# Optimization experiments

Hardware: AMD Instinct MI355X
Metric: run time of the kernel (lower is better)

Reference implementation:

```python
import jax, jax.numpy as jnp
import numpy as np

PATCH_NUM = 10  # self.patch_num divisor
TOP_N = 5


def _extract_patches(feat, ps):
    """feat: [1,C,H,W] -> [P, C*ps*ps] with P = (H-ps)*(W-ps), matching the
    original loop over h in range(H-ps), w in range(W-ps)."""
    C, H, W = feat.shape[1:]
    Hm, Wm = H - ps, W - ps
    shifts = [feat[0, :, i:i + Hm, j:j + Wm] for i in range(ps) for j in range(ps)]
    patches = jnp.stack(shifts, axis=1)          # [C, ps*ps, Hm, Wm]
    return patches.reshape(C * ps * ps, Hm * Wm).T  # [P, K], P index = h*Wm + w


def _scale_loss(src_f, tgt_f, pos, ps):
    C = src_f.shape[1]
    K = C * ps * ps
    patches = _extract_patches(src_f, ps)  # [P, K]

    def per_target(p):
        th, tw = p[0], p[1]
        tpatch = jax.lax.dynamic_slice(tgt_f, (0, 0, th, tw), (1, C, ps, ps)).reshape(K)
        dist = jnp.sum(jnp.abs(patches - tpatch), axis=1)  # [P] summed L1 per patch
        _, ids = jax.lax.top_k(-dist, TOP_N)                # 5 nearest patches
        sel = patches[ids]                                   # [TOP_N, K]
        # sum over top-n of mean-L1, each divided by top_n (as in original)
        return jnp.sum(jnp.mean(jnp.abs(sel - tpatch), axis=1)) / TOP_N

    # sequential map over the small number of target patches keeps peak memory
    # at one [P,K] abs-diff buffer per step
    return jnp.sum(jax.lax.map(per_target, pos))


def setup_inputs() -> dict:
    key = jax.random.key(0)
    k0, k1, k2, k3, k4, k5 = jax.random.split(key, 6)
    return {
        "src_f0": jax.random.normal(k0, (1, 64, 256, 256), dtype=jnp.float32),
        "tgt_f0": jax.random.normal(k1, (1, 64, 256, 256), dtype=jnp.float32),
        "src_f1": jax.random.normal(k2, (1, 128, 128, 128), dtype=jnp.float32),
        "tgt_f1": jax.random.normal(k3, (1, 128, 128, 128), dtype=jnp.float32),
        "pos0": jax.random.randint(k4, (10, 2), 0, 253, dtype=jnp.int32),
        "pos1": jax.random.randint(k5, (5, 2), 0, 127, dtype=jnp.int32),
    }


def reference(src_f0, tgt_f0, src_f1, tgt_f1, pos0, pos1):
    loss = _scale_loss(src_f0, tgt_f0, pos0, 3) + _scale_loss(src_f1, tgt_f1, pos1, 1)
    return loss / PATCH_NUM
```

## Files before the change

### kernel.cpp

```cpp
#include <hip/hip_runtime.h>
#include <hip/hip_bf16.h>

#define BIG 3.4e38f


__device__ __forceinline__ void merge5(float a[5], const float* b) {
    float r[5];
#pragma unroll
    for (int k = 0; k < 5; ++k) {
        float best = BIG;
#pragma unroll
        for (int i = 0; i <= k + 1; ++i) {
            const int j = k + 1 - i;
            float va = (i == 0) ? -BIG : a[i - 1];
            float vb = (j == 0) ? -BIG : b[j - 1];
            best = fminf(best, fmaxf(va, vb));
        }
        r[k] = best;
    }
#pragma unroll
    for (int k = 0; k < 5; ++k) a[k] = r[k];
}

__device__ __forceinline__ void top5_insert(float m[5], float d) {
    if (d < m[4]) {
        m[4] = d;
#pragma unroll
        for (int k = 4; k > 0; --k) {
            float lo = fminf(m[k - 1], m[k]);
            float hi = fmaxf(m[k - 1], m[k]);
            m[k - 1] = lo;
            m[k] = hi;
        }
    }
}

__device__ __forceinline__ void wave_merge_top5(float m[5]) {
#pragma unroll
    for (int off = 1; off < 64; off <<= 1) {
        float o[5];
#pragma unroll
        for (int k = 0; k < 5; ++k) o[k] = __shfl_xor(m[k], off, 64);
        merge5(m, o);
    }
}

__device__ __forceinline__ bool block_merge_top5(float m[5], float (*s_top)[5],
                                                 float r[5]) {
    const int wid = threadIdx.x >> 6;
    if ((threadIdx.x & 63) == 0) {
#pragma unroll
        for (int k = 0; k < 5; ++k) s_top[wid][k] = m[k];
    }
    __syncthreads();
    if (threadIdx.x == 0) {
#pragma unroll
        for (int k = 0; k < 5; ++k) r[k] = s_top[0][k];
        merge5(r, s_top[1]);
        merge5(r, s_top[2]);
        merge5(r, s_top[3]);
        return true;
    }
    return false;
}

__global__ __launch_bounds__(256) void dist_all_kernel(
    const float* __restrict__ src0, const float* __restrict__ tgt0,
    const int* __restrict__ pos0, const float* __restrict__ src1,
    const float* __restrict__ tgt1, const int* __restrict__ pos1,
    float* __restrict__ dist0, float* __restrict__ p2b) {
    __shared__ float tl[960];
    __shared__ float s_top[4][5];

    if (blockIdx.y < 8) {
        constexpr int H = 256, W = 256, HW = H * W, T = 10, CCH = 8;
        constexpr int PLANE = 253 * 256;
        const int c0 = blockIdx.y * CCH;

        for (int idx = threadIdx.x; idx < T * CCH * 9; idx += 256) {
            int t = idx / (CCH * 9);
            int rem = idx - t * (CCH * 9);
            int cc = rem / 9;
            int r2 = rem - cc * 9;
            int i = r2 / 3, j = r2 - i * 3;
            int th = pos0[2 * t], tw = pos0[2 * t + 1];
            tl[((t * CCH + cc) * 3 + i) * 4 + j] =
                tgt0[(size_t)(c0 + cc) * HW + (th + i) * W + (tw + j)];
        }
        __syncthreads();

        const int tx = threadIdx.x & 63;
        const int ty = threadIdx.x >> 6;
        const int h = blockIdx.x * 4 + ty;
        const int hl = (h <= 250) ? h : 250;
        const int w0 = tx * 4;
        const int bw = (w0 <= 248) ? w0 + 4 : 248;

        float acc[T][4];
#pragma unroll
        for (int t = 0; t < T; ++t)
#pragma unroll
            for (int n = 0; n < 4; ++n) acc[t][n] = 0.f;

        const float* sb = src0 + (size_t)c0 * HW + hl * W;
        for (int cc = 0; cc < CCH; ++cc) {
            const float* row0 = sb + (size_t)cc * HW;
#pragma unroll
            for (int i = 0; i < 3; ++i) {
                const float4 a = *(const float4*)(row0 + i * W + w0);
                const float2 b = *(const float2*)(row0 + i * W + bw);
                const float r[6] = {a.x, a.y, a.z, a.w, b.x, b.y};
#pragma unroll
                for (int t = 0; t < T; ++t) {
                    const float4 tv =
                        *(const float4*)&tl[((t * CCH + cc) * 3 + i) * 4];
#pragma unroll
                    for (int n = 0; n < 4; ++n)
                        acc[t][n] += fabsf(r[n] - tv.x) +
                                     fabsf(r[n + 1] - tv.y) +
                                     fabsf(r[n + 2] - tv.z);
                }
            }
        }

        if (h < 253) {
            float* dp = dist0 + (size_t)blockIdx.y * T * PLANE + h * 256 + w0;
#pragma unroll
            for (int t = 0; t < T; ++t) {
                float4 o = {acc[t][0], acc[t][1], acc[t][2], acc[t][3]};
                *(float4*)(dp + (size_t)t * PLANE) = o;
            }
        }
    } else {
        constexpr int H = 128, W = 128, HW = H * W, T = 5, C = 128;
        for (int idx = threadIdx.x; idx < T * C; idx += 256) {
            int t = idx / C, cc = idx - t * C;
            tl[idx] =
                tgt1[(size_t)cc * HW + pos1[2 * t] * W + pos1[2 * t + 1]];
        }
        __syncthreads();

        const int w = threadIdx.x & 127;
        const int h = blockIdx.x * 2 + (threadIdx.x >> 7);
        float acc[T] = {0.f, 0.f, 0.f, 0.f, 0.f};
        const float* sp = src1 + h * W + w;
        for (int cc = 0; cc < C; ++cc) {
            const float v = sp[(size_t)cc * HW];
#pragma unroll
            for (int t = 0; t < T; ++t) acc[t] += fabsf(v - tl[t * C + cc]);
        }
        const bool valid = (h < 127) && (w < 127);
#pragma unroll
        for (int t = 0; t < T; ++t) {
            float m[5] = {valid ? acc[t] : BIG, BIG, BIG, BIG, BIG};
            wave_merge_top5(m);
            float r[5];
            if (block_merge_top5(m, s_top, r)) {
                float* dst = p2b + (t * 64 + blockIdx.x) * 5;
#pragma unroll
                for (int k = 0; k < 5; ++k) dst[k] = r[k];
            }
            __syncthreads();
        }
    }
}

template <int PLANE, int ROWW, int VALIDW, int NCH, int T, int NB>
__global__ __launch_bounds__(256) void top5_stage_kernel(
    const float* __restrict__ dist, float* __restrict__ part2) {
    __shared__ float s_top[4][5];
    const int t = blockIdx.y;
    constexpr int NF = PLANE / 4;
    constexpr int ITERS = (NF + NB * 256 - 1) / (NB * 256);
    float m[5] = {BIG, BIG, BIG, BIG, BIG};
#pragma unroll
    for (int k = 0; k < ITERS; ++k) {
        const int f = blockIdx.x * (ITERS * 256) + k * 256 + threadIdx.x;
        if (f < NF) {
            float4 s = *(const float4*)&dist[(size_t)t * PLANE + f * 4];
#pragma unroll
            for (int ch = 1; ch < NCH; ++ch) {
                float4 u =
                    *(const float4*)&dist[((size_t)ch * T + t) * PLANE + f * 4];
                s.x += u.x; s.y += u.y; s.z += u.z; s.w += u.w;
            }
            const int w0 = (f * 4) & (ROWW - 1);
            top5_insert(m, (w0 + 0 < VALIDW) ? s.x : BIG);
            top5_insert(m, (w0 + 1 < VALIDW) ? s.y : BIG);
            top5_insert(m, (w0 + 2 < VALIDW) ? s.z : BIG);
            top5_insert(m, (w0 + 3 < VALIDW) ? s.w : BIG);
        }
    }
    wave_merge_top5(m);
    float r[5];
    if (block_merge_top5(m, s_top, r)) {
        float* dst = part2 + (t * NB + blockIdx.x) * 5;
#pragma unroll
        for (int k = 0; k < 5; ++k) dst[k] = r[k];
    }
}

__global__ __launch_bounds__(256) void final_merge_kernel(
    const float* __restrict__ p2a, int na,
    const float* __restrict__ p2b, int nb,
    unsigned int* __restrict__ out) {
    __shared__ float s_sum[15];
    const int lane = threadIdx.x & 63;
    const int wv = threadIdx.x >> 6;
#pragma unroll
    for (int rt = 0; rt < 4; ++rt) {
        const int t = wv * 4 + rt;
        if (t < 15) {
            const float* base = (t < 10) ? p2a + t * na : p2b + (t - 10) * nb;
            const int n = (t < 10) ? na : nb;
            const float scale =
                (t < 10) ? 1.f / (576.f * 5.f) : 1.f / (128.f * 5.f);
            float m[5] = {BIG, BIG, BIG, BIG, BIG};
            for (int b0 = 0; b0 < n; b0 += 64)
                if (b0 + lane < n) top5_insert(m, base[b0 + lane]);
            wave_merge_top5(m);
            if (lane == 0)
                s_sum[t] = (m[0] + m[1] + m[2] + m[3] + m[4]) * scale;
        }
    }
    __syncthreads();
    if (threadIdx.x == 0) {
        float total = 0.f;
#pragma unroll
        for (int t = 0; t < 15; ++t) total += s_sum[t];
        union { float f; unsigned int i; } uf;
        uf.f = total * 0.1f;
        unsigned int bf = (uf.i + 0x7FFFu + ((uf.i >> 16) & 1u)) >> 16;
        out[0] = (uf.i & 0xFFFF0000u) | (bf & 0xFFFFu);
    }
}

template <int C, int H, int PS, int WM>
__global__ __launch_bounds__(256) void dist_top5_kernel(
    const float* __restrict__ src, const float* __restrict__ tgt,
    const int* __restrict__ pos, float* __restrict__ part) {
    constexpr int W = H;
    constexpr int K = C * PS * PS;
    constexpr int P = WM * WM;
    __shared__ float tlv[K];
    __shared__ float s_top[4][5];
    const int t = blockIdx.y;
    const int th = pos[2 * t], tw = pos[2 * t + 1];
    for (int idx = threadIdx.x; idx < K; idx += 256) {
        int c = idx / (PS * PS);
        int rem = idx - c * PS * PS;
        int i = rem / PS, j = rem - i * PS;
        tlv[idx] = tgt[(c * H + th + i) * W + tw + j];
    }
    __syncthreads();
    const int p = blockIdx.x * 256 + threadIdx.x;
    float d = BIG;
    if (p < P) {
        const int h = p / WM, w = p - h * WM;
        float acc = 0.f;
        for (int c = 0; c < C; ++c)
#pragma unroll
            for (int i = 0; i < PS; ++i) {
                const float* r = src + (c * H + h + i) * W + w;
                const float* tr = &tlv[(c * PS + i) * PS];
#pragma unroll
                for (int j = 0; j < PS; ++j) acc += fabsf(r[j] - tr[j]);
            }
        d = acc;
    }
    float m[5] = {d, BIG, BIG, BIG, BIG};
    wave_merge_top5(m);
    float r[5];
    if (block_merge_top5(m, s_top, r)) {
        float* dst = part + (t * gridDim.x + blockIdx.x) * 5;
#pragma unroll
        for (int k = 0; k < 5; ++k) dst[k] = r[k];
    }
}

extern "C" void kernel_launch(void* const* d_in, const int* in_sizes, int n_in,
                              void* d_out, int out_size, void* d_ws, size_t ws_size,
                              hipStream_t stream) {
    const float* src0 = (const float*)d_in[0];
    const float* tgt0 = (const float*)d_in[1];
    const float* src1 = (const float*)d_in[2];
    const float* tgt1 = (const float*)d_in[3];
    const int* pos0 = (const int*)d_in[4];
    const int* pos1 = (const int*)d_in[5];
    unsigned int* out = (unsigned int*)d_out;

    constexpr size_t PLANE0 = 253 * 256;
    constexpr size_t NP2A = 10 * 16 * 5;
    constexpr size_t NP2B = 5 * 64 * 5;
    const size_t need = (8 * 10 * PLANE0 + NP2A + NP2B) * 4;

    if (ws_size >= need) {
        float* dist0 = (float*)d_ws;
        float* p2a = dist0 + 8 * 10 * PLANE0;
        float* p2b = p2a + NP2A;

        dist_all_kernel<<<dim3(64, 9), 256, 0, stream>>>(
            src0, tgt0, pos0, src1, tgt1, pos1, dist0, p2b);
        top5_stage_kernel<253 * 256, 256, 253, 8, 10, 16>
            <<<dim3(16, 10), 256, 0, stream>>>(dist0, p2a);
        final_merge_kernel<<<dim3(1), 256, 0, stream>>>(p2a, 80, p2b, 320, out);
    } else {
        float* part0 = (float*)d_ws;
        float* part1 = part0 + 10 * 251 * 5;
        dist_top5_kernel<64, 256, 3, 253>
            <<<dim3(251, 10), 256, 0, stream>>>(src0, tgt0, pos0, part0);
        dist_top5_kernel<128, 128, 1, 127>
            <<<dim3(64, 5), 256, 0, stream>>>(src1, tgt1, pos1, part1);
        final_merge_kernel<<<dim3(1), 256, 0, stream>>>(part0, 1255, part1, 320, out);
    }
}
```

Before: 132.3 us.

## Split scale-0 distance work per target into many more blocks with scalar target values

The scale-0 distance kernel now assigns one target and one 8-channel chunk per block, growing the grid from 64x9 to 512x11 blocks. Each block keeps only 72 target values and moves them into uniform registers via readfirstlane, so the arithmetic can use scalar operands instead of LDS reads. This is meant to raise occupancy and parallelism on the many-CU GPU. The cost is that every source tile is now re-read from global memory (or L2) ten times, once per target, instead of once. The surplus scale-1 blocks return early.

```diff
diff --git a/kernel.cpp b/kernel.cpp
--- a/kernel.cpp
+++ b/kernel.cpp
@@ -2,6 +2,10 @@
 #include <hip/hip_bf16.h>
 
 #define BIG 3.4e38f
+
+__device__ __forceinline__ float uniform_f(float x) {
+    return __int_as_float(__builtin_amdgcn_readfirstlane(__float_as_int(x)));
+}
 
 
 __device__ __forceinline__ void merge5(float a[5], const float* b) {
@@ -69,69 +73,64 @@
     const int* __restrict__ pos0, const float* __restrict__ src1,
     const float* __restrict__ tgt1, const int* __restrict__ pos1,
     float* __restrict__ dist0, float* __restrict__ p2b) {
-    __shared__ float tl[960];
+    __shared__ float tl[640];
     __shared__ float s_top[4][5];
 
-    if (blockIdx.y < 8) {
-        constexpr int H = 256, W = 256, HW = H * W, T = 10, CCH = 8;
+    if (blockIdx.y < 10) {
+        constexpr int H = 256, W = 256, HW = H * W, CCH = 8;
         constexpr int PLANE = 253 * 256;
-        const int c0 = blockIdx.y * CCH;
-
-        for (int idx = threadIdx.x; idx < T * CCH * 9; idx += 256) {
-            int t = idx / (CCH * 9);
-            int rem = idx - t * (CCH * 9);
-            int cc = rem / 9;
-            int r2 = rem - cc * 9;
-            int i = r2 / 3, j = r2 - i * 3;
-            int th = pos0[2 * t], tw = pos0[2 * t + 1];
-            tl[((t * CCH + cc) * 3 + i) * 4 + j] =
+        const int t = blockIdx.y;
+        const int chunk = blockIdx.x & 7;
+        const int hg = blockIdx.x >> 3;
+        const int c0 = chunk * CCH;
+
+        if (threadIdx.x < 72) {
+            const int cc = threadIdx.x / 9;
+            const int r2 = threadIdx.x - cc * 9;
+            const int i = r2 / 3, j = r2 - i * 3;
+            const int th = pos0[2 * t], tw = pos0[2 * t + 1];
+            tl[threadIdx.x] =
                 tgt0[(size_t)(c0 + cc) * HW + (th + i) * W + (tw + j)];
         }
         __syncthreads();
+
+        float tv[72];
+#pragma unroll
+        for (int k = 0; k < 72; ++k) tv[k] = uniform_f(tl[k]);
 
         const int tx = threadIdx.x & 63;
         const int ty = threadIdx.x >> 6;
-        const int h = blockIdx.x * 4 + ty;
-        const int hl = (h <= 250) ? h : 250;
+        const int h = hg * 4 + ty;
+        const int hl = (h <= 252) ? h : 252;
         const int w0 = tx * 4;
         const int bw = (w0 <= 248) ? w0 + 4 : 248;
 
-        float acc[T][4];
-#pragma unroll
-        for (int t = 0; t < T; ++t)
-#pragma unroll
-            for (int n = 0; n < 4; ++n) acc[t][n] = 0.f;
-
-        const float* sb = src0 + (size_t)c0 * HW + hl * W;
+        float acc[4] = {0.f, 0.f, 0.f, 0.f};
+        const float* cbase = src0 + (size_t)c0 * HW + hl * W;
+#pragma unroll
         for (int cc = 0; cc < CCH; ++cc) {
-            const float* row0 = sb + (size_t)cc * HW;
+            const float* row = cbase + (size_t)cc * HW;
 #pragma unroll
             for (int i = 0; i < 3; ++i) {
-                const float4 a = *(const float4*)(row0 + i * W + w0);
-                const float2 b = *(const float2*)(row0 + i * W + bw);
+                const float4 a = *(const float4*)(row + i * W + w0);
+                const float2 b = *(const float2*)(row + i * W + bw);
                 const float r[6] = {a.x, a.y, a.z, a.w, b.x, b.y};
-#pragma unroll
-                for (int t = 0; t < T; ++t) {
-                    const float4 tv =
-                        *(const float4*)&tl[((t * CCH + cc) * 3 + i) * 4];
-#pragma unroll
-                    for (int n = 0; n < 4; ++n)
-                        acc[t][n] += fabsf(r[n] - tv.x) +
-                                     fabsf(r[n + 1] - tv.y) +
-                                     fabsf(r[n + 2] - tv.z);
-                }
+                const int kb = cc * 9 + i * 3;
+#pragma unroll
+                for (int n = 0; n < 4; ++n)
+                    acc[n] += fabsf(r[n] - tv[kb]) +
+                              fabsf(r[n + 1] - tv[kb + 1]) +
+                              fabsf(r[n + 2] - tv[kb + 2]);
             }
         }
 
         if (h < 253) {
-            float* dp = dist0 + (size_t)blockIdx.y * T * PLANE + h * 256 + w0;
-#pragma unroll
-            for (int t = 0; t < T; ++t) {
-                float4 o = {acc[t][0], acc[t][1], acc[t][2], acc[t][3]};
-                *(float4*)(dp + (size_t)t * PLANE) = o;
-            }
+            float4 o = {acc[0], acc[1], acc[2], acc[3]};
+            *(float4*)(dist0 + ((size_t)chunk * 10 + t) * PLANE + h * 256 +
+                       w0) = o;
         }
     } else {
+        if (blockIdx.x >= 64) return;
         constexpr int H = 128, W = 128, HW = H * W, T = 5, C = 128;
         for (int idx = threadIdx.x; idx < T * C; idx += 256) {
             int t = idx / C, cc = idx - t * C;
@@ -299,7 +298,7 @@
         float* p2a = dist0 + 8 * 10 * PLANE0;
         float* p2b = p2a + NP2A;
 
-        dist_all_kernel<<<dim3(64, 9), 256, 0, stream>>>(
+        dist_all_kernel<<<dim3(512, 11), 256, 0, stream>>>(
             src0, tgt0, pos0, src1, tgt1, pos1, dist0, p2b);
         top5_stage_kernel<253 * 256, 256, 253, 8, 10, 16>
             <<<dim3(16, 10), 256, 0, stream>>>(dist0, p2a);
```

After: 163.5 us. 1.24x slower.
